# Kernel optimization log

Measured on AMD Instinct MI355X. Metric: run time of the kernel, lower is better.

## Reference

```python
import jax, jax.numpy as jnp
import numpy as np

N_NODES = 50000
N_EDGES = 800000
D_IN = 128
D_OUT = 128
N_GRAPHS = 64
NEG_SLOPE = 0.01  # torch F.leaky_relu default


def gcn_conv(x, W, b, src, dst, n_nodes):
    """PyG GCNConv: linear, add self-loops, symmetric norm, scatter-add, bias."""
    h = x @ W  # [N, D_OUT]
    # degree including self-loop (edge_weight = 1)
    deg = jnp.zeros((n_nodes,), x.dtype).at[dst].add(1.0) + 1.0
    dinv = jax.lax.rsqrt(deg)
    norm = dinv[src] * dinv[dst]           # [E]
    agg = jnp.zeros_like(h).at[dst].add(h[src] * norm[:, None])
    # self-loop contribution: dinv[i]*dinv[i]*h[i] = h[i]/deg[i]
    return agg + h * (1.0 / deg)[:, None] + b


def gcn_branch(x, edge_index, Ws, bs):
    src, dst = edge_index[0], edge_index[1]
    n = x.shape[0]
    for W, b in zip(Ws, bs):
        x = gcn_conv(x, W, b, src, dst, n)
        x = jax.nn.leaky_relu(x, NEG_SLOPE)
        # dropout is identity in eval mode
    return x


def mean_pool(x, batch, num_graphs):
    s = jax.ops.segment_sum(x, batch, num_segments=num_graphs)
    cnt = jax.ops.segment_sum(jnp.ones((x.shape[0],), x.dtype), batch, num_segments=num_graphs)
    return s / jnp.maximum(cnt, 1.0)[:, None]


def setup_inputs() -> dict:
    key = jax.random.key(0)
    ks = jax.random.split(key, 20)
    inp = {
        'x1': jax.random.normal(ks[0], (N_NODES, D_IN), jnp.float32),
        'edge_index1': jax.random.randint(ks[1], (2, N_EDGES), 0, N_NODES, jnp.int64 if jax.config.jax_enable_x64 else jnp.int32),
        'batch1': jnp.sort(jax.random.randint(ks[2], (N_NODES,), 0, N_GRAPHS)),
        'x2': jax.random.normal(ks[3], (N_NODES, D_IN), jnp.float32),
        'edge_index2': jax.random.randint(ks[4], (2, N_EDGES), 0, N_NODES, jnp.int64 if jax.config.jax_enable_x64 else jnp.int32),
        'batch2': jnp.sort(jax.random.randint(ks[5], (N_NODES,), 0, N_GRAPHS)),
    }
    s = 1.0 / np.sqrt(D_IN)
    inp['W1_0'] = jax.random.uniform(ks[6], (D_IN, D_OUT), jnp.float32, -s, s)
    inp['b1_0'] = jnp.zeros((D_OUT,), jnp.float32)
    inp['W1_1'] = jax.random.uniform(ks[7], (D_OUT, D_OUT), jnp.float32, -s, s)
    inp['b1_1'] = jnp.zeros((D_OUT,), jnp.float32)
    inp['W2_0'] = jax.random.uniform(ks[8], (D_IN, D_OUT), jnp.float32, -s, s)
    inp['b2_0'] = jnp.zeros((D_OUT,), jnp.float32)
    inp['W2_1'] = jax.random.uniform(ks[9], (D_OUT, D_OUT), jnp.float32, -s, s)
    inp['b2_1'] = jnp.zeros((D_OUT,), jnp.float32)
    s2 = 1.0 / np.sqrt(2 * D_OUT)
    inp['lin1_W'] = jax.random.uniform(ks[10], (2 * D_OUT, D_OUT), jnp.float32, -s2, s2)
    inp['lin1_b'] = jax.random.uniform(ks[11], (D_OUT,), jnp.float32, -s2, s2)
    s3 = 1.0 / np.sqrt(D_OUT)
    inp['lin2_W'] = jax.random.uniform(ks[12], (D_OUT, 1), jnp.float32, -s3, s3)
    inp['lin2_b'] = jax.random.uniform(ks[13], (1,), jnp.float32, -s3, s3)
    return inp


def reference(x1, edge_index1, batch1, x2, edge_index2, batch2,
              W1_0, b1_0, W1_1, b1_1, W2_0, b2_0, W2_1, b2_1,
              lin1_W, lin1_b, lin2_W, lin2_b):
    h1 = gcn_branch(x1, edge_index1, [W1_0, W1_1], [b1_0, b1_1])
    h1 = mean_pool(h1, batch1, N_GRAPHS)
    h2 = gcn_branch(x2, edge_index2, [W2_0, W2_1], [b2_0, b2_1])
    h2 = mean_pool(h2, batch2, N_GRAPHS)
    h = jnp.concatenate([h1, h2], axis=-1)  # [G, 256]
    h = jax.nn.relu(h @ lin1_W + lin1_b)
    return h @ lin2_W + lin2_b  # [G, 1]
```

## Files before the change

kernel.cpp:

```cpp
#include <hip/hip_runtime.h>
#include <hip/hip_fp16.h>

#define N_NODES 50000
#define N_EDGES 800000
#define D 128
#define N_GRAPHS 64
#define NEG_SLOPE 0.01f
#define POOL_PARTS 8
#define ELLW 32
#define OVF_CAP 8192

#define BUCKETS 196
#define NPAD (BUCKETS * 256)
#define EPB 4096
#define BCAP 5120

typedef _Float16 half8 __attribute__((ext_vector_type(8)));
typedef _Float16 half4 __attribute__((ext_vector_type(4)));
typedef float f32x4 __attribute__((ext_vector_type(4)));
typedef float f32x2 __attribute__((ext_vector_type(2)));

__global__ __launch_bounds__(256) void k_prep(const float* __restrict__ Wa, const float* __restrict__ Wb,
                                              const float* __restrict__ Wc, const float* __restrict__ Wd,
                                              __half* __restrict__ WtH) {
    const float* Ws[4] = {Wa, Wb, Wc, Wd};
    const float* W = Ws[blockIdx.x];
    __half* o = WtH + (size_t)blockIdx.x * 16384;
    int t = threadIdx.x;
    for (int r = 0; r < 64; r++) {
        int e = r * 256 + t;
        int k = e >> 7, n = e & 127;
        o[n * 128 + k] = __float2half(W[k * 128 + n]);
    }
}

__global__ __launch_bounds__(256) void k_part(const int* __restrict__ ei1, const int* __restrict__ ei2,
                                              int* __restrict__ gcnt, int2* __restrict__ bucketed) {
    const int br = blockIdx.y;
    const int* __restrict__ src = (br ? ei2 : ei1);
    const int* __restrict__ dst = src + N_EDGES;
    int* __restrict__ gc = gcnt + br * BUCKETS;
    int2* __restrict__ bk = bucketed + (size_t)br * BUCKETS * BCAP;

    __shared__ int bcnt[BUCKETS];
    __shared__ int bofs[BUCKETS];
    __shared__ int gbase[BUCKETS];
    __shared__ int2 stage[EPB];
    const int tid = threadIdx.x;
    const int base = blockIdx.x * EPB;
    for (int b = tid; b < BUCKETS; b += 256) bcnt[b] = 0;
    __syncthreads();
    int d_[16], s_[16], p_[16];
#pragma unroll
    for (int k = 0; k < 16; k++) {
        int i = base + k * 256 + tid;
        bool v = i < N_EDGES;
        d_[k] = v ? dst[i] : -1;
        s_[k] = v ? src[i] : 0;
        p_[k] = 0;
        if (v) p_[k] = atomicAdd(&bcnt[d_[k] >> 8], 1);
    }
    __syncthreads();
    if (tid == 0) {
        int run = 0;
        for (int b = 0; b < BUCKETS; b++) { bofs[b] = run; run += bcnt[b]; }
    }
    __syncthreads();
    if (tid < BUCKETS) gbase[tid] = atomicAdd(&gc[tid], bcnt[tid]);
    __syncthreads();
#pragma unroll
    for (int k = 0; k < 16; k++) {
        if (d_[k] >= 0) stage[bofs[d_[k] >> 8] + p_[k]] = make_int2(d_[k], s_[k]);
    }
    __syncthreads();
    int total = bofs[BUCKETS - 1] + bcnt[BUCKETS - 1];
    for (int i = tid; i < total; i += 256) {
        int2 e = stage[i];
        int b = e.x >> 8;
        int dest = gbase[b] + (i - bofs[b]);
        if (dest < BCAP) bk[(size_t)b * BCAP + dest] = e;
    }
}

__global__ __launch_bounds__(256) void k_build(const int* __restrict__ gcnt, const int2* __restrict__ bucketed,
                                               int* __restrict__ cnti, unsigned short* __restrict__ ell,
                                               int2* __restrict__ ovf, int* __restrict__ ocnt) {
    const int br = blockIdx.y;
    const int* __restrict__ gc = gcnt + br * BUCKETS;
    const int2* __restrict__ bk = bucketed + (size_t)br * BUCKETS * BCAP;
    int* __restrict__ ci = cnti + br * NPAD;
    unsigned short* __restrict__ el = ell + (size_t)br * NPAD * ELLW;
    int2* __restrict__ ov = ovf + (size_t)br * OVF_CAP;
    int* __restrict__ oc = ocnt + br;

    __shared__ unsigned short lell[256 * ELLW];
    __shared__ int lcnt[256];
    const int b = blockIdx.x, tid = threadIdx.x;
    lcnt[tid] = 0;
    __syncthreads();
    int nb = min(gc[b], BCAP);
    const int2* __restrict__ bp = bk + (size_t)b * BCAP;
    for (int i = tid; i < nb; i += 256) {
        int2 e = bp[i];
        int dl = e.x & 255;
        int p = atomicAdd(&lcnt[dl], 1);
        if (p < ELLW) {
            lell[dl * ELLW + p] = (unsigned short)e.y;
        } else {
            int o = atomicAdd(oc, 1);
            if (o < OVF_CAP) ov[o] = e;
        }
    }
    __syncthreads();
    ci[b * 256 + tid] = lcnt[tid];
    uint4* eg = (uint4*)(el + (size_t)b * 256 * ELLW);
    const uint4* elc = (const uint4*)lell;
    for (int i = tid; i < 256 * ELLW * 2 / 16; i += 256) eg[i] = elc[i];
}

#define XS 136
template <bool FP16IN>
__global__ __launch_bounds__(256) void k_gemm(const void* __restrict__ xin1, const void* __restrict__ xin2,
                                              const __half* __restrict__ WtHall, int layer,
                                              const int* __restrict__ cnti, unsigned char* __restrict__ H8) {
    const int br = blockIdx.y;
    const void* __restrict__ xin = (br ? xin2 : xin1);
    const __half* __restrict__ WtH = WtHall + (size_t)(br * 2 + layer) * 16384;
    const int* __restrict__ cnt = cnti + br * NPAD;
    unsigned char* __restrict__ h = H8 + (size_t)br * N_NODES * 128;

    __shared__ _Float16 Xl[64 * XS];
    __shared__ _Float16 Wt[128 * XS];
    const int tid = threadIdx.x;
    const int w = tid >> 6, lane = tid & 63;
    const int quad = lane >> 4, l16 = lane & 15;
    const int row0 = blockIdx.x * 64;

#pragma unroll
    for (int i = 0; i < 8; i++) {
        int i2 = tid + 256 * i;
        int r = i2 >> 4, cg = i2 & 15;
        *(uint4*)&Wt[r * XS + cg * 8] = ((const uint4*)WtH)[i2];
    }
    if (FP16IN) {
        const __half* x = (const __half*)xin;
#pragma unroll
        for (int i = 0; i < 4; i++) {
            int i2 = tid + 256 * i;
            int r = i2 >> 4, cg = i2 & 15;
            uint4 v = make_uint4(0, 0, 0, 0);
            if (row0 + r < N_NODES) v = ((const uint4*)(x + (size_t)(row0 + r) * D))[cg];
            *(uint4*)&Xl[r * XS + cg * 8] = v;
        }
    } else {
        const float* x = (const float*)xin;
#pragma unroll
        for (int i = 0; i < 8; i++) {
            int i2 = tid + 256 * i;
            int r = i2 >> 5, f4 = i2 & 31;
            float4 v = make_float4(0.f, 0.f, 0.f, 0.f);
            if (row0 + r < N_NODES) v = *(const float4*)((const float*)x + (size_t)(row0 + r) * D + f4 * 4);
            half4 hv;
            hv[0] = (_Float16)v.x; hv[1] = (_Float16)v.y; hv[2] = (_Float16)v.z; hv[3] = (_Float16)v.w;
            *(half4*)&Xl[r * XS + f4 * 4] = hv;
        }
    }
    __syncthreads();

    half8 a[4];
#pragma unroll
    for (int kb = 0; kb < 4; kb++)
        a[kb] = *(const half8*)&Xl[(w * 16 + l16) * XS + kb * 32 + quad * 8];

    const int rbase = row0 + w * 16 + quad * 4;
    float di[4];
#pragma unroll
    for (int reg = 0; reg < 4; reg++) {
        int r = rbase + reg;
        di[reg] = (r < N_NODES) ? rsqrtf((float)cnt[r] + 1.0f) : 0.0f;
    }

    float accs[8][4];
#pragma unroll
    for (int ct = 0; ct < 8; ct++) {
        f32x4 acc = {0.f, 0.f, 0.f, 0.f};
#pragma unroll
        for (int kb = 0; kb < 4; kb++) {
            half8 b = *(const half8*)&Wt[(ct * 16 + l16) * XS + kb * 32 + quad * 8];
            acc = __builtin_amdgcn_mfma_f32_16x16x32_f16(a[kb], b, acc, 0, 0, 0);
        }
#pragma unroll
        for (int reg = 0; reg < 4; reg++) accs[ct][reg] = acc[reg] * di[reg];
    }

    __syncthreads();
    unsigned char* S = (unsigned char*)Xl;
#pragma unroll
    for (int ct = 0; ct < 8; ct++)
#pragma unroll
        for (int reg = 0; reg < 4; reg++) {
            int p = __builtin_amdgcn_cvt_pk_fp8_f32(accs[ct][reg], accs[ct][reg], 0, false);
            S[(w * 16 + quad * 4 + reg) * 128 + ct * 16 + l16] = (unsigned char)p;
        }
    __syncthreads();
#pragma unroll
    for (int i = 0; i < 2; i++) {
        int idx = tid + 256 * i;
        int r = idx >> 3, cg = idx & 7;
        if (row0 + r < N_NODES)
            ((uint4*)(h + (size_t)(row0 + r) * 128))[cg] = ((const uint4*)S)[idx];
    }
}

__global__ __launch_bounds__(256) void k_agg(const int* __restrict__ cnti, const unsigned short* __restrict__ ell,
                                             const int2* __restrict__ ovf, const int* __restrict__ ocnt,
                                             const unsigned char* __restrict__ H8all, const float* __restrict__ bias1,
                                             const float* __restrict__ bias2, __half* __restrict__ ACT) {
    const int br = blockIdx.y;
    const int* __restrict__ cnt = cnti + br * NPAD;
    const unsigned short* __restrict__ el = ell + (size_t)br * NPAD * ELLW;
    const int2* __restrict__ ov = ovf + (size_t)br * OVF_CAP;
    const unsigned char* __restrict__ H8 = H8all + (size_t)br * N_NODES * 128;
    const float* __restrict__ bias = (br ? bias2 : bias1);
    __half* __restrict__ out = ACT + (size_t)br * N_NODES * D;

    const int tid = threadIdx.x;
    const int l32 = tid & 31;
    const int node = blockIdx.x * 8 + (tid >> 5);
    int n = cnt[node];
    int nc = min(n, ELLW);
    int sv = 0;
    if (l32 < nc) sv = (int)el[(size_t)node * ELLW + l32];
    int ncOther = __shfl(nc, (tid & 63) ^ 32, 64);
    int jmax = max(nc, ncOther);

    float4 acc[8];
    {
        unsigned int dw = *(const unsigned int*)(H8 + (size_t)node * 128 + l32 * 4);
        f32x2 lo = __builtin_amdgcn_cvt_pk_f32_fp8((int)dw, false);
        f32x2 hi = __builtin_amdgcn_cvt_pk_f32_fp8((int)dw, true);
        acc[0] = make_float4(lo[0], lo[1], hi[0], hi[1]);
    }
#pragma unroll
    for (int i = 1; i < 8; i++) acc[i] = make_float4(0.f, 0.f, 0.f, 0.f);

    for (int j = 0; j < jmax; j += 8) {
        int s[8]; float w[8];
#pragma unroll
        for (int i = 0; i < 8; i++) {
            s[i] = __shfl(sv, j + i, 32);
            w[i] = ((j + i) < nc) ? 1.0f : 0.0f;
        }
#pragma unroll
        for (int i = 0; i < 8; i++) {
            unsigned int dw = *(const unsigned int*)(H8 + (size_t)s[i] * 128 + l32 * 4);
            f32x2 lo = __builtin_amdgcn_cvt_pk_f32_fp8((int)dw, false);
            f32x2 hi = __builtin_amdgcn_cvt_pk_f32_fp8((int)dw, true);
            acc[i].x = fmaf(w[i], lo[0], acc[i].x);
            acc[i].y = fmaf(w[i], lo[1], acc[i].y);
            acc[i].z = fmaf(w[i], hi[0], acc[i].z);
            acc[i].w = fmaf(w[i], hi[1], acc[i].w);
        }
    }
    if (n > ELLW) {
        int oc = min(ocnt[br], OVF_CAP);
        for (int o = 0; o < oc; o++) {
            int2 p = ov[o];
            if (p.x == node) {
                unsigned int dw = *(const unsigned int*)(H8 + (size_t)p.y * 128 + l32 * 4);
                f32x2 lo = __builtin_amdgcn_cvt_pk_f32_fp8((int)dw, false);
                f32x2 hi = __builtin_amdgcn_cvt_pk_f32_fp8((int)dw, true);
                acc[0].x += lo[0]; acc[0].y += lo[1]; acc[0].z += hi[0]; acc[0].w += hi[1];
            }
        }
    }
    float sx = ((acc[0].x + acc[1].x) + (acc[2].x + acc[3].x)) + ((acc[4].x + acc[5].x) + (acc[6].x + acc[7].x));
    float sy = ((acc[0].y + acc[1].y) + (acc[2].y + acc[3].y)) + ((acc[4].y + acc[5].y) + (acc[6].y + acc[7].y));
    float sz = ((acc[0].z + acc[1].z) + (acc[2].z + acc[3].z)) + ((acc[4].z + acc[5].z) + (acc[6].z + acc[7].z));
    float sw = ((acc[0].w + acc[1].w) + (acc[2].w + acc[3].w)) + ((acc[4].w + acc[5].w) + (acc[6].w + acc[7].w));
    float dv = rsqrtf((float)n + 1.0f);
    float4 b = ((const float4*)bias)[l32];
    float vx = sx * dv + b.x;
    float vy = sy * dv + b.y;
    float vz = sz * dv + b.z;
    float vw = sw * dv + b.w;
    vx = vx > 0.0f ? vx : NEG_SLOPE * vx;
    vy = vy > 0.0f ? vy : NEG_SLOPE * vy;
    vz = vz > 0.0f ? vz : NEG_SLOPE * vz;
    vw = vw > 0.0f ? vw : NEG_SLOPE * vw;
    union { __half2 h2[2]; uint2 u; } up;
    up.h2[0] = __floats2half2_rn(vx, vy);
    up.h2[1] = __floats2half2_rn(vz, vw);
    *(uint2*)(out + (size_t)node * 128 + l32 * 4) = up.u;
}

__device__ __forceinline__ int lower_bound_i(const int* __restrict__ arr, int n, int key) {
    int lo = 0, hi = n;
    while (lo < hi) {
        int mid = (lo + hi) >> 1;
        if (arr[mid] < key) lo = mid + 1; else hi = mid;
    }
    return lo;
}

__global__ __launch_bounds__(256) void k_pool(const __half* __restrict__ ACT, const int* __restrict__ batch1,
                                              const int* __restrict__ batch2, float* __restrict__ ppall,
                                              float* __restrict__ cntall) {
    const int br = blockIdx.z;
    const __half* __restrict__ h = ACT + (size_t)br * N_NODES * D;
    const int* __restrict__ batch = (br ? batch2 : batch1);
    float* __restrict__ pp = ppall + (size_t)br * N_GRAPHS * POOL_PARTS * D;
    float* __restrict__ cnt = cntall + br * N_GRAPHS;

    int g = blockIdx.x;
    int part = blockIdx.y;
    int lo = lower_bound_i(batch, N_NODES, g);
    int hi = lower_bound_i(batch, N_NODES, g + 1);
    int num = hi - lo;
    if (part == 0 && threadIdx.x == 0) cnt[g] = (float)num;
    int chunk = (num + POOL_PARTS - 1) / POOL_PARTS;
    int a = lo + part * chunk;
    int b = min(a + chunk, hi);
    int c2 = threadIdx.x & 63;
    int sub = threadIdx.x >> 6;
    const __half2* __restrict__ h2 = (const __half2*)h;
    float2 acc = make_float2(0.f, 0.f);
    for (int node = a + sub; node < b; node += 4) {
        float2 v = __half22float2(h2[(size_t)node * 64 + c2]);
        acc.x += v.x; acc.y += v.y;
    }
    __shared__ float2 tmp[256];
    tmp[threadIdx.x] = acc;
    __syncthreads();
    if (sub == 0) {
        float2 s;
        s.x = tmp[c2].x + tmp[c2 + 64].x + tmp[c2 + 128].x + tmp[c2 + 192].x;
        s.y = tmp[c2].y + tmp[c2 + 64].y + tmp[c2 + 128].y + tmp[c2 + 192].y;
        ((float2*)pp)[((size_t)g * POOL_PARTS + part) * 64 + c2] = s;
    }
}

__global__ __launch_bounds__(128) void k_mlp(const float* __restrict__ pp1, const float* __restrict__ pp2,
                                             const float* __restrict__ cnt1, const float* __restrict__ cnt2,
                                             const float* __restrict__ lin1W, const float* __restrict__ lin1b,
                                             const float* __restrict__ lin2W, const float* __restrict__ lin2b,
                                             float* __restrict__ out) {
    int g = blockIdx.x;
    int c = threadIdx.x;
    __shared__ float cat[2 * D];
    float s1 = 0.f, s2 = 0.f;
#pragma unroll
    for (int p = 0; p < POOL_PARTS; p++) {
        s1 += pp1[((size_t)g * POOL_PARTS + p) * D + c];
        s2 += pp2[((size_t)g * POOL_PARTS + p) * D + c];
    }
    cat[c] = s1 / fmaxf(cnt1[g], 1.0f);
    cat[c + D] = s2 / fmaxf(cnt2[g], 1.0f);
    __syncthreads();
    float acc = lin1b[c];
#pragma unroll 8
    for (int k = 0; k < 2 * D; k++) acc += cat[k] * lin1W[k * D + c];
    acc = fmaxf(acc, 0.0f);
    float v = acc * lin2W[c];
#pragma unroll
    for (int off = 32; off > 0; off >>= 1) v += __shfl_down(v, off, 64);
    __shared__ float wsum[2];
    if ((c & 63) == 0) wsum[c >> 6] = v;
    __syncthreads();
    if (c == 0) out[g] = wsum[0] + wsum[1] + lin2b[0];
}

extern "C" void kernel_launch(void* const* d_in, const int* in_sizes, int n_in,
                              void* d_out, int out_size, void* d_ws, size_t ws_size,
                              hipStream_t stream) {
    const float* x1 = (const float*)d_in[0];
    const int*   ei1 = (const int*)d_in[1];
    const int*   batch1 = (const int*)d_in[2];
    const float* x2 = (const float*)d_in[3];
    const int*   ei2 = (const int*)d_in[4];
    const int*   batch2 = (const int*)d_in[5];
    const float* W1_0 = (const float*)d_in[6];
    const float* b1_0 = (const float*)d_in[7];
    const float* W1_1 = (const float*)d_in[8];
    const float* b1_1 = (const float*)d_in[9];
    const float* W2_0 = (const float*)d_in[10];
    const float* b2_0 = (const float*)d_in[11];
    const float* W2_1 = (const float*)d_in[12];
    const float* b2_1 = (const float*)d_in[13];
    const float* lin1W = (const float*)d_in[14];
    const float* lin1b = (const float*)d_in[15];
    const float* lin2W = (const float*)d_in[16];
    const float* lin2b = (const float*)d_in[17];
    float* out = (float*)d_out;

    __half* WtH = (__half*)d_ws;
    __half* ACT = WtH + 65536;
    unsigned char* H8 = (unsigned char*)(ACT + 2 * (size_t)N_NODES * D);
    int*    cnti = (int*)(H8 + 2 * (size_t)N_NODES * 128);
    int*    gcnt = cnti + 2 * NPAD;
    int*    ocnt = gcnt + 2 * BUCKETS;
    int2*   ovf  = (int2*)(ocnt + 8);
    unsigned short* ell = (unsigned short*)(ovf + 2 * (size_t)OVF_CAP);
    int2*   bucketed = (int2*)(ell + 2 * (size_t)NPAD * ELLW);
    float*  pp  = (float*)(bucketed + 2 * (size_t)BUCKETS * BCAP);
    float*  cnt = pp + 2 * (size_t)N_GRAPHS * POOL_PARTS * D;

    dim3 b256(256);
    int partBlocks = (N_EDGES + EPB - 1) / EPB;
    int gemmBlocks = (N_NODES + 63) / 64;
    int aggBlocks  = N_NODES / 8;

    k_prep<<<4, b256, 0, stream>>>(W1_0, W1_1, W2_0, W2_1, WtH);
    hipMemsetAsync(gcnt, 0, (2 * BUCKETS + 8) * sizeof(int), stream);

    k_part <<<dim3(partBlocks, 2), b256, 0, stream>>>(ei1, ei2, gcnt, bucketed);
    k_build<<<dim3(BUCKETS, 2),    b256, 0, stream>>>(gcnt, bucketed, cnti, ell, ovf, ocnt);

    k_gemm<false><<<dim3(gemmBlocks, 2), b256, 0, stream>>>(x1, x2, WtH, 0, cnti, H8);
    k_agg        <<<dim3(aggBlocks, 2),  b256, 0, stream>>>(cnti, ell, ovf, ocnt, H8, b1_0, b2_0, ACT);
    k_gemm<true> <<<dim3(gemmBlocks, 2), b256, 0, stream>>>(ACT, ACT + (size_t)N_NODES * D, WtH, 1, cnti, H8);
    k_agg        <<<dim3(aggBlocks, 2),  b256, 0, stream>>>(cnti, ell, ovf, ocnt, H8, b1_1, b2_1, ACT);

    k_pool<<<dim3(N_GRAPHS, POOL_PARTS, 2), b256, 0, stream>>>(ACT, batch1, batch2, pp, cnt);

    k_mlp<<<N_GRAPHS, dim3(128), 0, stream>>>(pp, pp + (size_t)N_GRAPHS * POOL_PARTS * D,
                                              cnt, cnt + N_GRAPHS,
                                              lin1W, lin1b, lin2W, lin2b, out);
}
```

Before: 291.5 us.

## Fuse aggregation with next GEMM and with mean pooling; fold memset into prep

Result: slower. 312.0 us (+7.0%).

```diff
diff --git a/kernel.cpp b/kernel.cpp
--- a/kernel.cpp
+++ b/kernel.cpp
@@ -6,7 +6,6 @@
 #define D 128
 #define N_GRAPHS 64
 #define NEG_SLOPE 0.01f
-#define POOL_PARTS 8
 #define ELLW 32
 #define OVF_CAP 8192
 
@@ -14,15 +13,27 @@
 #define NPAD (BUCKETS * 256)
 #define EPB 4096
 #define BCAP 5120
+#define XS 136
 
 typedef _Float16 half8 __attribute__((ext_vector_type(8)));
 typedef _Float16 half4 __attribute__((ext_vector_type(4)));
 typedef float f32x4 __attribute__((ext_vector_type(4)));
 typedef float f32x2 __attribute__((ext_vector_type(2)));
 
+__device__ __forceinline__ int lower_bound_i(const int* __restrict__ arr, int n, int key) {
+    int lo = 0, hi = n;
+    while (lo < hi) {
+        int mid = (lo + hi) >> 1;
+        if (arr[mid] < key) lo = mid + 1; else hi = mid;
+    }
+    return lo;
+}
+
 __global__ __launch_bounds__(256) void k_prep(const float* __restrict__ Wa, const float* __restrict__ Wb,
                                               const float* __restrict__ Wc, const float* __restrict__ Wd,
-                                              __half* __restrict__ WtH) {
+                                              const int* __restrict__ batch1, const int* __restrict__ batch2,
+                                              __half* __restrict__ WtH, int* __restrict__ gcnt,
+                                              float* __restrict__ pp, int* __restrict__ cntg) {
     const float* Ws[4] = {Wa, Wb, Wc, Wd};
     const float* W = Ws[blockIdx.x];
     __half* o = WtH + (size_t)blockIdx.x * 16384;
@@ -32,6 +43,17 @@
         int k = e >> 7, n = e & 127;
         o[n * 128 + k] = __float2half(W[k * 128 + n]);
     }
+#pragma unroll
+    for (int i = 0; i < 16; i++) pp[blockIdx.x * 4096 + i * 256 + t] = 0.0f;
+    if (blockIdx.x == 0) {
+        for (int i = t; i < 2 * BUCKETS + 8; i += 256) gcnt[i] = 0;
+    }
+    if (blockIdx.x == 1) {
+        if (t < 64)
+            cntg[t] = lower_bound_i(batch1, N_NODES, t + 1) - lower_bound_i(batch1, N_NODES, t);
+        else if (t < 128)
+            cntg[t] = lower_bound_i(batch2, N_NODES, (t - 64) + 1) - lower_bound_i(batch2, N_NODES, t - 64);
+    }
 }
 
 __global__ __launch_bounds__(256) void k_part(const int* __restrict__ ei1, const int* __restrict__ ei2,
@@ -45,6 +67,8 @@
     __shared__ int bcnt[BUCKETS];
     __shared__ int bofs[BUCKETS];
     __shared__ int gbase[BUCKETS];
+    __shared__ int sc[BUCKETS];
+    __shared__ int stot;
     __shared__ int2 stage[EPB];
     const int tid = threadIdx.x;
     const int base = blockIdx.x * EPB;
@@ -61,19 +85,26 @@
         if (v) p_[k] = atomicAdd(&bcnt[d_[k] >> 8], 1);
     }
     __syncthreads();
-    if (tid == 0) {
-        int run = 0;
-        for (int b = 0; b < BUCKETS; b++) { bofs[b] = run; run += bcnt[b]; }
-    }
-    __syncthreads();
-    if (tid < BUCKETS) gbase[tid] = atomicAdd(&gc[tid], bcnt[tid]);
+    if (tid < BUCKETS) sc[tid] = bcnt[tid];
+    __syncthreads();
+    for (int off = 1; off < BUCKETS; off <<= 1) {
+        int v = (tid < BUCKETS && tid >= off) ? sc[tid - off] : 0;
+        __syncthreads();
+        if (tid < BUCKETS) sc[tid] += v;
+        __syncthreads();
+    }
+    if (tid < BUCKETS) {
+        bofs[tid] = sc[tid] - bcnt[tid];
+        gbase[tid] = atomicAdd(&gc[tid], bcnt[tid]);
+    }
+    if (tid == BUCKETS - 1) stot = sc[tid];
     __syncthreads();
 #pragma unroll
     for (int k = 0; k < 16; k++) {
         if (d_[k] >= 0) stage[bofs[d_[k] >> 8] + p_[k]] = make_int2(d_[k], s_[k]);
     }
     __syncthreads();
-    int total = bofs[BUCKETS - 1] + bcnt[BUCKETS - 1];
+    int total = stot;
     for (int i = tid; i < total; i += 256) {
         int2 e = stage[i];
         int b = e.x >> 8;
@@ -118,14 +149,12 @@
     for (int i = tid; i < 256 * ELLW * 2 / 16; i += 256) eg[i] = elc[i];
 }
 
-#define XS 136
-template <bool FP16IN>
-__global__ __launch_bounds__(256) void k_gemm(const void* __restrict__ xin1, const void* __restrict__ xin2,
-                                              const __half* __restrict__ WtHall, int layer,
+__global__ __launch_bounds__(256) void k_gemm(const float* __restrict__ x1, const float* __restrict__ x2,
+                                              const __half* __restrict__ WtHall,
                                               const int* __restrict__ cnti, unsigned char* __restrict__ H8) {
     const int br = blockIdx.y;
-    const void* __restrict__ xin = (br ? xin2 : xin1);
-    const __half* __restrict__ WtH = WtHall + (size_t)(br * 2 + layer) * 16384;
+    const float* __restrict__ x = (br ? x2 : x1);
+    const __half* __restrict__ WtH = WtHall + (size_t)(br * 2 + 0) * 16384;
     const int* __restrict__ cnt = cnti + br * NPAD;
     unsigned char* __restrict__ h = H8 + (size_t)br * N_NODES * 128;
 
@@ -142,28 +171,15 @@
         int r = i2 >> 4, cg = i2 & 15;
         *(uint4*)&Wt[r * XS + cg * 8] = ((const uint4*)WtH)[i2];
     }
-    if (FP16IN) {
-        const __half* x = (const __half*)xin;
-#pragma unroll
-        for (int i = 0; i < 4; i++) {
-            int i2 = tid + 256 * i;
-            int r = i2 >> 4, cg = i2 & 15;
-            uint4 v = make_uint4(0, 0, 0, 0);
-            if (row0 + r < N_NODES) v = ((const uint4*)(x + (size_t)(row0 + r) * D))[cg];
-            *(uint4*)&Xl[r * XS + cg * 8] = v;
-        }
-    } else {
-        const float* x = (const float*)xin;
-#pragma unroll
-        for (int i = 0; i < 8; i++) {
-            int i2 = tid + 256 * i;
-            int r = i2 >> 5, f4 = i2 & 31;
-            float4 v = make_float4(0.f, 0.f, 0.f, 0.f);
-            if (row0 + r < N_NODES) v = *(const float4*)((const float*)x + (size_t)(row0 + r) * D + f4 * 4);
-            half4 hv;
-            hv[0] = (_Float16)v.x; hv[1] = (_Float16)v.y; hv[2] = (_Float16)v.z; hv[3] = (_Float16)v.w;
-            *(half4*)&Xl[r * XS + f4 * 4] = hv;
-        }
+#pragma unroll
+    for (int i = 0; i < 8; i++) {
+        int i2 = tid + 256 * i;
+        int r = i2 >> 5, f4 = i2 & 31;
+        float4 v = make_float4(0.f, 0.f, 0.f, 0.f);
+        if (row0 + r < N_NODES) v = *(const float4*)(x + (size_t)(row0 + r) * D + f4 * 4);
+        half4 hv;
+        hv[0] = (_Float16)v.x; hv[1] = (_Float16)v.y; hv[2] = (_Float16)v.z; hv[3] = (_Float16)v.w;
+        *(half4*)&Xl[r * XS + f4 * 4] = hv;
     }
     __syncthreads();
 
@@ -212,21 +228,177 @@
     }
 }
 
-__global__ __launch_bounds__(256) void k_agg(const int* __restrict__ cnti, const unsigned short* __restrict__ ell,
-                                             const int2* __restrict__ ovf, const int* __restrict__ ocnt,
-                                             const unsigned char* __restrict__ H8all, const float* __restrict__ bias1,
-                                             const float* __restrict__ bias2, __half* __restrict__ ACT) {
+__global__ __launch_bounds__(256) void k_aggemm(const int* __restrict__ cnti, const unsigned short* __restrict__ ell,
+                                                const int2* __restrict__ ovf, const int* __restrict__ ocnt,
+                                                const unsigned char* __restrict__ H8in,
+                                                const float* __restrict__ bias1, const float* __restrict__ bias2,
+                                                const __half* __restrict__ WtHall,
+                                                unsigned char* __restrict__ H8out) {
+    const int br = blockIdx.y;
+    const int* __restrict__ cnt = cnti + br * NPAD;
+    const unsigned short* __restrict__ el = ell + (size_t)br * NPAD * ELLW;
+    const int2* __restrict__ ov = ovf + (size_t)br * OVF_CAP;
+    const unsigned char* __restrict__ H8 = H8in + (size_t)br * N_NODES * 128;
+    const float* __restrict__ bias = (br ? bias2 : bias1);
+    const __half* __restrict__ WtH = WtHall + (size_t)(br * 2 + 1) * 16384;
+    unsigned char* __restrict__ hout = H8out + (size_t)br * N_NODES * 128;
+
+    __shared__ _Float16 Xl[64 * XS];
+    __shared__ _Float16 Wt[128 * XS];
+    const int tid = threadIdx.x;
+    const int w = tid >> 6, lane = tid & 63;
+    const int quad = lane >> 4, l16 = lane & 15;
+    const int l32 = tid & 31;
+    const int hw = tid >> 5;
+    const int row0 = blockIdx.x * 64;
+
+#pragma unroll
+    for (int i = 0; i < 8; i++) {
+        int i2 = tid + 256 * i;
+        int r = i2 >> 4, cg = i2 & 15;
+        *(uint4*)&Wt[r * XS + cg * 8] = ((const uint4*)WtH)[i2];
+    }
+
+    float4 bv = ((const float4*)bias)[l32];
+    for (int t = 0; t < 8; t++) {
+        const int r = hw * 8 + t;
+        const int node = row0 + r;
+        const bool valid = node < N_NODES;
+        int n = valid ? cnt[node] : 0;
+        int nc = min(n, ELLW);
+        int sv = 0;
+        if (l32 < nc) sv = (int)el[(size_t)node * ELLW + l32];
+
+        float4 acc[8];
+        if (valid) {
+            unsigned int dw = *(const unsigned int*)(H8 + (size_t)node * 128 + l32 * 4);
+            f32x2 lo = __builtin_amdgcn_cvt_pk_f32_fp8((int)dw, false);
+            f32x2 hi = __builtin_amdgcn_cvt_pk_f32_fp8((int)dw, true);
+            acc[0] = make_float4(lo[0], lo[1], hi[0], hi[1]);
+        } else {
+            acc[0] = make_float4(0.f, 0.f, 0.f, 0.f);
+        }
+#pragma unroll
+        for (int i = 1; i < 8; i++) acc[i] = make_float4(0.f, 0.f, 0.f, 0.f);
+
+        for (int j = 0; j < nc; j += 8) {
+            int s[8]; float wt[8];
+#pragma unroll
+            for (int i = 0; i < 8; i++) {
+                s[i] = __shfl(sv, j + i, 32);
+                wt[i] = ((j + i) < nc) ? 1.0f : 0.0f;
+            }
+#pragma unroll
+            for (int i = 0; i < 8; i++) {
+                unsigned int dw = *(const unsigned int*)(H8 + (size_t)s[i] * 128 + l32 * 4);
+                f32x2 lo = __builtin_amdgcn_cvt_pk_f32_fp8((int)dw, false);
+                f32x2 hi = __builtin_amdgcn_cvt_pk_f32_fp8((int)dw, true);
+                acc[i].x = fmaf(wt[i], lo[0], acc[i].x);
+                acc[i].y = fmaf(wt[i], lo[1], acc[i].y);
+                acc[i].z = fmaf(wt[i], hi[0], acc[i].z);
+                acc[i].w = fmaf(wt[i], hi[1], acc[i].w);
+            }
+        }
+        if (n > ELLW) {
+            int oc = min(ocnt[br], OVF_CAP);
+            for (int o = 0; o < oc; o++) {
+                int2 p = ov[o];
+                if (p.x == node) {
+                    unsigned int dw = *(const unsigned int*)(H8 + (size_t)p.y * 128 + l32 * 4);
+                    f32x2 lo = __builtin_amdgcn_cvt_pk_f32_fp8((int)dw, false);
+                    f32x2 hi = __builtin_amdgcn_cvt_pk_f32_fp8((int)dw, true);
+                    acc[0].x += lo[0]; acc[0].y += lo[1]; acc[0].z += hi[0]; acc[0].w += hi[1];
+                }
+            }
+        }
+        float sx = ((acc[0].x + acc[1].x) + (acc[2].x + acc[3].x)) + ((acc[4].x + acc[5].x) + (acc[6].x + acc[7].x));
+        float sy = ((acc[0].y + acc[1].y) + (acc[2].y + acc[3].y)) + ((acc[4].y + acc[5].y) + (acc[6].y + acc[7].y));
+        float sz = ((acc[0].z + acc[1].z) + (acc[2].z + acc[3].z)) + ((acc[4].z + acc[5].z) + (acc[6].z + acc[7].z));
+        float sw = ((acc[0].w + acc[1].w) + (acc[2].w + acc[3].w)) + ((acc[4].w + acc[5].w) + (acc[6].w + acc[7].w));
+        float dv = rsqrtf((float)n + 1.0f);
+        float vx = sx * dv + bv.x;
+        float vy = sy * dv + bv.y;
+        float vz = sz * dv + bv.z;
+        float vw = sw * dv + bv.w;
+        vx = vx > 0.0f ? vx : NEG_SLOPE * vx;
+        vy = vy > 0.0f ? vy : NEG_SLOPE * vy;
+        vz = vz > 0.0f ? vz : NEG_SLOPE * vz;
+        vw = vw > 0.0f ? vw : NEG_SLOPE * vw;
+        union { __half2 h2[2]; uint2 u; } up;
+        if (valid) {
+            up.h2[0] = __floats2half2_rn(vx, vy);
+            up.h2[1] = __floats2half2_rn(vz, vw);
+        } else {
+            up.u = make_uint2(0u, 0u);
+        }
+        *(uint2*)&Xl[r * XS + l32 * 4] = up.u;
+    }
+    __syncthreads();
+
+    half8 a[4];
+#pragma unroll
+    for (int kb = 0; kb < 4; kb++)
+        a[kb] = *(const half8*)&Xl[(w * 16 + l16) * XS + kb * 32 + quad * 8];
+
+    const int rbase = row0 + w * 16 + quad * 4;
+    float di[4];
+#pragma unroll
+    for (int reg = 0; reg < 4; reg++) {
+        int r = rbase + reg;
+        di[reg] = (r < N_NODES) ? rsqrtf((float)cnt[r] + 1.0f) : 0.0f;
+    }
+
+    float accs[8][4];
+#pragma unroll
+    for (int ct = 0; ct < 8; ct++) {
+        f32x4 acc = {0.f, 0.f, 0.f, 0.f};
+#pragma unroll
+        for (int kb = 0; kb < 4; kb++) {
+            half8 b = *(const half8*)&Wt[(ct * 16 + l16) * XS + kb * 32 + quad * 8];
+            acc = __builtin_amdgcn_mfma_f32_16x16x32_f16(a[kb], b, acc, 0, 0, 0);
+        }
+#pragma unroll
+        for (int reg = 0; reg < 4; reg++) accs[ct][reg] = acc[reg] * di[reg];
+    }
+
+    __syncthreads();
+    unsigned char* S = (unsigned char*)Xl;
+#pragma unroll
+    for (int ct = 0; ct < 8; ct++)
+#pragma unroll
+        for (int reg = 0; reg < 4; reg++) {
+            int p = __builtin_amdgcn_cvt_pk_fp8_f32(accs[ct][reg], accs[ct][reg], 0, false);
+            S[(w * 16 + quad * 4 + reg) * 128 + ct * 16 + l16] = (unsigned char)p;
+        }
+    __syncthreads();
+#pragma unroll
+    for (int i = 0; i < 2; i++) {
+        int idx = tid + 256 * i;
+        int r = idx >> 3, cg = idx & 7;
+        if (row0 + r < N_NODES)
+            ((uint4*)(hout + (size_t)(row0 + r) * 128))[cg] = ((const uint4*)S)[idx];
+    }
+}
+
+__global__ __launch_bounds__(256) void k_aggpool(const int* __restrict__ cnti, const unsigned short* __restrict__ ell,
+                                                 const int2* __restrict__ ovf, const int* __restrict__ ocnt,
+                                                 const unsigned char* __restrict__ H8all,
+                                                 const float* __restrict__ bias1, const float* __restrict__ bias2,
+                                                 const int* __restrict__ batch1, const int* __restrict__ batch2,
+                                                 float* __restrict__ ppall) {
     const int br = blockIdx.y;
     const int* __restrict__ cnt = cnti + br * NPAD;
     const unsigned short* __restrict__ el = ell + (size_t)br * NPAD * ELLW;
     const int2* __restrict__ ov = ovf + (size_t)br * OVF_CAP;
     const unsigned char* __restrict__ H8 = H8all + (size_t)br * N_NODES * 128;
     const float* __restrict__ bias = (br ? bias2 : bias1);
-    __half* __restrict__ out = ACT + (size_t)br * N_NODES * D;
+    const int* __restrict__ batch = (br ? batch2 : batch1);
+    float* __restrict__ pp = ppall + (size_t)br * N_GRAPHS * D;
 
     const int tid = threadIdx.x;
     const int l32 = tid & 31;
-    const int node = blockIdx.x * 8 + (tid >> 5);
+    const int hw = tid >> 5;
+    const int node = blockIdx.x * 8 + hw;
     int n = cnt[node];
     int nc = min(n, ELLW);
     int sv = 0;
@@ -245,21 +417,21 @@
     for (int i = 1; i < 8; i++) acc[i] = make_float4(0.f, 0.f, 0.f, 0.f);
 
     for (int j = 0; j < jmax; j += 8) {
-        int s[8]; float w[8];
+        int s[8]; float wt[8];
 #pragma unroll
         for (int i = 0; i < 8; i++) {
             s[i] = __shfl(sv, j + i, 32);
-            w[i] = ((j + i) < nc) ? 1.0f : 0.0f;
+            wt[i] = ((j + i) < nc) ? 1.0f : 0.0f;
         }
 #pragma unroll
         for (int i = 0; i < 8; i++) {
             unsigned int dw = *(const unsigned int*)(H8 + (size_t)s[i] * 128 + l32 * 4);
             f32x2 lo = __builtin_amdgcn_cvt_pk_f32_fp8((int)dw, false);
             f32x2 hi = __builtin_amdgcn_cvt_pk_f32_fp8((int)dw, true);
-            acc[i].x = fmaf(w[i], lo[0], acc[i].x);
-            acc[i].y = fmaf(w[i], lo[1], acc[i].y);
-            acc[i].z = fmaf(w[i], hi[0], acc[i].z);
-            acc[i].w = fmaf(w[i], hi[1], acc[i].w);
+            acc[i].x = fmaf(wt[i], lo[0], acc[i].x);
+            acc[i].y = fmaf(wt[i], lo[1], acc[i].y);
+            acc[i].z = fmaf(wt[i], hi[0], acc[i].z);
+            acc[i].w = fmaf(wt[i], hi[1], acc[i].w);
         }
     }
     if (n > ELLW) {
@@ -288,74 +460,41 @@
     vy = vy > 0.0f ? vy : NEG_SLOPE * vy;
     vz = vz > 0.0f ? vz : NEG_SLOPE * vz;
     vw = vw > 0.0f ? vw : NEG_SLOPE * vw;
-    union { __half2 h2[2]; uint2 u; } up;
-    up.h2[0] = __floats2half2_rn(vx, vy);
-    up.h2[1] = __floats2half2_rn(vz, vw);
-    *(uint2*)(out + (size_t)node * 128 + l32 * 4) = up.u;
-}
-
-__device__ __forceinline__ int lower_bound_i(const int* __restrict__ arr, int n, int key) {
-    int lo = 0, hi = n;
-    while (lo < hi) {
-        int mid = (lo + hi) >> 1;
-        if (arr[mid] < key) lo = mid + 1; else hi = mid;
-    }
-    return lo;
-}
-
-__global__ __launch_bounds__(256) void k_pool(const __half* __restrict__ ACT, const int* __restrict__ batch1,
-                                              const int* __restrict__ batch2, float* __restrict__ ppall,
-                                              float* __restrict__ cntall) {
-    const int br = blockIdx.z;
-    const __half* __restrict__ h = ACT + (size_t)br * N_NODES * D;
-    const int* __restrict__ batch = (br ? batch2 : batch1);
-    float* __restrict__ pp = ppall + (size_t)br * N_GRAPHS * POOL_PARTS * D;
-    float* __restrict__ cnt = cntall + br * N_GRAPHS;
-
-    int g = blockIdx.x;
-    int part = blockIdx.y;
-    int lo = lower_bound_i(batch, N_NODES, g);
-    int hi = lower_bound_i(batch, N_NODES, g + 1);
-    int num = hi - lo;
-    if (part == 0 && threadIdx.x == 0) cnt[g] = (float)num;
-    int chunk = (num + POOL_PARTS - 1) / POOL_PARTS;
-    int a = lo + part * chunk;
-    int b = min(a + chunk, hi);
-    int c2 = threadIdx.x & 63;
-    int sub = threadIdx.x >> 6;
-    const __half2* __restrict__ h2 = (const __half2*)h;
-    float2 acc = make_float2(0.f, 0.f);
-    for (int node = a + sub; node < b; node += 4) {
-        float2 v = __half22float2(h2[(size_t)node * 64 + c2]);
-        acc.x += v.x; acc.y += v.y;
-    }
-    __shared__ float2 tmp[256];
-    tmp[threadIdx.x] = acc;
-    __syncthreads();
-    if (sub == 0) {
-        float2 s;
-        s.x = tmp[c2].x + tmp[c2 + 64].x + tmp[c2 + 128].x + tmp[c2 + 192].x;
-        s.y = tmp[c2].y + tmp[c2 + 64].y + tmp[c2 + 128].y + tmp[c2 + 192].y;
-        ((float2*)pp)[((size_t)g * POOL_PARTS + part) * 64 + c2] = s;
-    }
-}
-
-__global__ __launch_bounds__(128) void k_mlp(const float* __restrict__ pp1, const float* __restrict__ pp2,
-                                             const float* __restrict__ cnt1, const float* __restrict__ cnt2,
+    __half2 q0 = __floats2half2_rn(vx, vy);
+    __half2 q1 = __floats2half2_rn(vz, vw);
+    float2 f0 = __half22float2(q0);
+    float2 f1 = __half22float2(q1);
+
+    __shared__ float sacc[8][128];
+    __shared__ int sg[8];
+    *(float4*)&sacc[hw][l32 * 4] = make_float4(f0.x, f0.y, f1.x, f1.y);
+    if (l32 == 0) sg[hw] = batch[node];
+    __syncthreads();
+    if (tid < 128) {
+        float s = sacc[0][tid];
+        int g = sg[0];
+        for (int r2 = 1; r2 < 8; r2++) {
+            if (sg[r2] == g) {
+                s += sacc[r2][tid];
+            } else {
+                atomicAdd(&pp[(size_t)g * D + tid], s);
+                s = sacc[r2][tid];
+                g = sg[r2];
+            }
+        }
+        atomicAdd(&pp[(size_t)g * D + tid], s);
+    }
+}
+
+__global__ __launch_bounds__(128) void k_mlp(const float* __restrict__ pp, const int* __restrict__ cntg,
                                              const float* __restrict__ lin1W, const float* __restrict__ lin1b,
                                              const float* __restrict__ lin2W, const float* __restrict__ lin2b,
                                              float* __restrict__ out) {
     int g = blockIdx.x;
     int c = threadIdx.x;
     __shared__ float cat[2 * D];
-    float s1 = 0.f, s2 = 0.f;
-#pragma unroll
-    for (int p = 0; p < POOL_PARTS; p++) {
-        s1 += pp1[((size_t)g * POOL_PARTS + p) * D + c];
-        s2 += pp2[((size_t)g * POOL_PARTS + p) * D + c];
-    }
-    cat[c] = s1 / fmaxf(cnt1[g], 1.0f);
-    cat[c + D] = s2 / fmaxf(cnt2[g], 1.0f);
+    cat[c] = pp[(size_t)g * D + c] / fmaxf((float)cntg[g], 1.0f);
+    cat[c + D] = pp[(size_t)(N_GRAPHS + g) * D + c] / fmaxf((float)cntg[64 + g], 1.0f);
     __syncthreads();
     float acc = lin1b[c];
 #pragma unroll 8
@@ -394,36 +533,30 @@
     float* out = (float*)d_out;
 
     __half* WtH = (__half*)d_ws;
-    __half* ACT = WtH + 65536;
-    unsigned char* H8 = (unsigned char*)(ACT + 2 * (size_t)N_NODES * D);
-    int*    cnti = (int*)(H8 + 2 * (size_t)N_NODES * 128);
+    unsigned char* H8a = (unsigned char*)(WtH + 65536);
+    unsigned char* H8b = H8a + 2 * (size_t)N_NODES * 128;
+    unsigned short* ell = (unsigned short*)(H8b + 2 * (size_t)N_NODES * 128);
+    int2*   bucketed = (int2*)(ell + 2 * (size_t)NPAD * ELLW);
+    int*    cnti = (int*)(bucketed + 2 * (size_t)BUCKETS * BCAP);
     int*    gcnt = cnti + 2 * NPAD;
     int*    ocnt = gcnt + 2 * BUCKETS;
-    int2*   ovf  = (int2*)(ocnt + 8);
-    unsigned short* ell = (unsigned short*)(ovf + 2 * (size_t)OVF_CAP);
-    int2*   bucketed = (int2*)(ell + 2 * (size_t)NPAD * ELLW);
-    float*  pp  = (float*)(bucketed + 2 * (size_t)BUCKETS * BCAP);
-    float*  cnt = pp + 2 * (size_t)N_GRAPHS * POOL_PARTS * D;
+    int*    cntg = ocnt + 8;
+    int2*   ovf  = (int2*)(cntg + 128);
+    float*  pp   = (float*)(ovf + 2 * (size_t)OVF_CAP);
 
     dim3 b256(256);
     int partBlocks = (N_EDGES + EPB - 1) / EPB;
     int gemmBlocks = (N_NODES + 63) / 64;
     int aggBlocks  = N_NODES / 8;
 
-    k_prep<<<4, b256, 0, stream>>>(W1_0, W1_1, W2_0, W2_1, WtH);
-    hipMemsetAsync(gcnt, 0, (2 * BUCKETS + 8) * sizeof(int), stream);
-
-    k_part <<<dim3(partBlocks, 2), b256, 0, stream>>>(ei1, ei2, gcnt, bucketed);
-    k_build<<<dim3(BUCKETS, 2),    b256, 0, stream>>>(gcnt, bucketed, cnti, ell, ovf, ocnt);
-
-    k_gemm<false><<<dim3(gemmBlocks, 2), b256, 0, stream>>>(x1, x2, WtH, 0, cnti, H8);
-    k_agg        <<<dim3(aggBlocks, 2),  b256, 0, stream>>>(cnti, ell, ovf, ocnt, H8, b1_0, b2_0, ACT);
-    k_gemm<true> <<<dim3(gemmBlocks, 2), b256, 0, stream>>>(ACT, ACT + (size_t)N_NODES * D, WtH, 1, cnti, H8);
-    k_agg        <<<dim3(aggBlocks, 2),  b256, 0, stream>>>(cnti, ell, ovf, ocnt, H8, b1_1, b2_1, ACT);
-
-    k_pool<<<dim3(N_GRAPHS, POOL_PARTS, 2), b256, 0, stream>>>(ACT, batch1, batch2, pp, cnt);
-
-    k_mlp<<<N_GRAPHS, dim3(128), 0, stream>>>(pp, pp + (size_t)N_GRAPHS * POOL_PARTS * D,
-                                              cnt, cnt + N_GRAPHS,
-                                              lin1W, lin1b, lin2W, lin2b, out);
-}
+    k_prep<<<4, b256, 0, stream>>>(W1_0, W1_1, W2_0, W2_1, batch1, batch2, WtH, gcnt, pp, cntg);
+
+    k_part  <<<dim3(partBlocks, 2), b256, 0, stream>>>(ei1, ei2, gcnt, bucketed);
+    k_build <<<dim3(BUCKETS, 2),    b256, 0, stream>>>(gcnt, bucketed, cnti, ell, ovf, ocnt);
+
+    k_gemm   <<<dim3(gemmBlocks, 2), b256, 0, stream>>>(x1, x2, WtH, cnti, H8a);
+    k_aggemm <<<dim3(gemmBlocks, 2), b256, 0, stream>>>(cnti, ell, ovf, ocnt, H8a, b1_0, b2_0, WtH, H8b);
+    k_aggpool<<<dim3(aggBlocks, 2),  b256, 0, stream>>>(cnti, ell, ovf, ocnt, H8b, b1_1, b2_1, batch1, batch2, pp);
+
+    k_mlp<<<N_GRAPHS, dim3(128), 0, stream>>>(pp, cntg, lin1W, lin1b, lin2W, lin2b, out);
+}
```
